# Performance work log

Hardware: AMD Instinct MI355X
Metric: run time of the kernel (lower is better)

## Reference

```python
import jax, jax.numpy as jnp
import numpy as np

EPS = 1e-5  # torch BatchNorm2d default


def _conv1x1(x, w):
    # x: [n, cin, h, w], w: [cout, cin] (1x1 conv == per-pixel matmul)
    return jnp.einsum('nchw,oc->nohw', x, w)


def _bn(x, gamma, beta, mean, var):
    # inference-mode BatchNorm2d over channel dim
    scale = gamma * jax.lax.rsqrt(var + EPS)
    shift = beta - mean * scale
    return x * scale[None, :, None, None] + shift[None, :, None, None]


def setup_inputs() -> dict:
    key = jax.random.key(0)
    ks = jax.random.split(key, 24)
    n, c, h, w = 16, 256, 64, 64
    width, planes = c // 2, c
    inp = {
        'x': jax.random.normal(ks[0], (n, c, h, w), jnp.float32),
        'w_theta': jax.random.normal(ks[1], (width, c), jnp.float32) * 0.05,
        'w_phi': jax.random.normal(ks[2], (width, c), jnp.float32) * 0.05,
        'w_g': jax.random.normal(ks[3], (width, c), jnp.float32) * 0.05,
        'w_zeta': jax.random.normal(ks[4], (planes, width), jnp.float32) * 0.05,
    }
    for i, (name, dim) in enumerate([('bn1', width), ('bn2', width), ('bn3', width), ('bn4', planes)]):
        k = 5 + 4 * i
        inp[f'{name}_gamma'] = jax.random.uniform(ks[k], (dim,), jnp.float32, 0.5, 1.5)
        inp[f'{name}_beta'] = jax.random.normal(ks[k + 1], (dim,), jnp.float32) * 0.1
        inp[f'{name}_mean'] = jax.random.normal(ks[k + 2], (dim,), jnp.float32) * 0.1
        inp[f'{name}_var'] = jax.random.uniform(ks[k + 3], (dim,), jnp.float32, 0.5, 1.5)
    return inp


def reference(x, w_theta, w_phi, w_g, w_zeta,
              bn1_gamma, bn1_beta, bn1_mean, bn1_var,
              bn2_gamma, bn2_beta, bn2_mean, bn2_var,
              bn3_gamma, bn3_beta, bn3_mean, bn3_var,
              bn4_gamma, bn4_beta, bn4_mean, bn4_var):
    n, c, h, w = x.shape
    theta = jax.nn.relu(_bn(_conv1x1(x, w_theta), bn1_gamma, bn1_beta, bn1_mean, bn1_var))
    phi = jax.nn.relu(_bn(_conv1x1(x, w_phi), bn2_gamma, bn2_beta, bn2_mean, bn2_var))
    g = jax.nn.relu(_bn(_conv1x1(x, w_g), bn3_gamma, bn3_beta, bn3_mean, bn3_var))

    width = theta.shape[1]
    hw = h * w
    theta = theta.reshape(n, width, hw)  # [n, C', S]
    phi = phi.reshape(n, width, hw)      # [n, C', S]
    g = g.reshape(n, width, hw)          # [n, C', S]

    # (theta^T @ phi) @ g^T == theta^T @ (phi @ g^T): no softmax, so associativity
    # lets us contract over pixels first -> O(S*C'^2) instead of O(S^2*C').
    kv = jnp.einsum('ncs,nds->ncd', phi, g)      # [n, C', C']
    out = jnp.einsum('ncs,ncd->nsd', theta, kv)  # [n, S, C']

    # faithful to torch: reshape (not transpose) [n, S, C'] -> [n, C', h, w]
    out = out.reshape(n, width, h, w)
    out = _bn(_conv1x1(out, w_zeta), bn4_gamma, bn4_beta, bn4_mean, bn4_var)
    return jax.nn.relu(out + x)
```

## Files before the change

### kernel.cpp

```cpp
#include <hip/hip_runtime.h>

#define BN_EPS 1e-5f

typedef unsigned short u16;
typedef __bf16 bf16x8 __attribute__((ext_vector_type(8)));
typedef float floatx4 __attribute__((ext_vector_type(4)));
typedef u16 u16x4 __attribute__((ext_vector_type(4)));
typedef u16 u16x8 __attribute__((ext_vector_type(8)));

__device__ __forceinline__ u16 f2bf(float f) {
    union { float f; unsigned int u; } v; v.f = f;
    unsigned int r = (v.u + 0x7fffu + ((v.u >> 16) & 1u)) >> 16;
    return (u16)r;
}

__device__ __forceinline__ void gld16(const void* gsrc, void* ldst) {
    __builtin_amdgcn_global_load_lds(
        (const __attribute__((address_space(1))) unsigned int*)gsrc,
        (__attribute__((address_space(3))) unsigned int*)ldst, 16, 0, 0);
}

__global__ __launch_bounds__(256) void prep_kernel(
    const float* __restrict__ wt, const float* __restrict__ wp,
    const float* __restrict__ wg, const float* __restrict__ wz,
    const float* __restrict__ g1, const float* __restrict__ b1,
    const float* __restrict__ m1, const float* __restrict__ v1,
    const float* __restrict__ g2, const float* __restrict__ b2,
    const float* __restrict__ m2, const float* __restrict__ v2,
    const float* __restrict__ g3, const float* __restrict__ b3,
    const float* __restrict__ m3, const float* __restrict__ v3,
    const float* __restrict__ g4, const float* __restrict__ b4,
    const float* __restrict__ m4, const float* __restrict__ v4,
    u16* __restrict__ W1bf, float* __restrict__ shift1,
    u16* __restrict__ Wzbf, float* __restrict__ shift4)
{
    int id = blockIdx.x * 256 + threadIdx.x;
    if (id < 384 * 256) {
        int r = id >> 8, c = id & 255;
        int grp = r >> 7, ch = r & 127;
        const float* wsrc = grp == 0 ? wt : (grp == 1 ? wp : wg);
        const float* gg = grp == 0 ? g1 : (grp == 1 ? g2 : g3);
        const float* bb = grp == 0 ? b1 : (grp == 1 ? b2 : b3);
        const float* mm = grp == 0 ? m1 : (grp == 1 ? m2 : m3);
        const float* vv = grp == 0 ? v1 : (grp == 1 ? v2 : v3);
        float scale = gg[ch] * rsqrtf(vv[ch] + BN_EPS);
        W1bf[id] = f2bf(wsrc[ch * 256 + c] * scale);
        if (c == 0) shift1[r] = bb[ch] - mm[ch] * scale;
    }
    if (id < 256 * 128) {
        int o = id >> 7;
        float scale = g4[o] * rsqrtf(v4[o] + BN_EPS);
        Wzbf[id] = f2bf(wz[id] * scale);
        if ((id & 127) == 0) shift4[o] = b4[o] - m4[o] * scale;
    }
}

__global__ __launch_bounds__(256) void xt_kernel(
    const float* __restrict__ x, u16* __restrict__ xt)
{
    const int stile = blockIdx.x, n = blockIdx.y;
    const int t = threadIdx.x;
    __shared__ __align__(16) u16 lds[64 * 256];

    const float* xb = x + (size_t)n * 1048576 + stile * 64;
    const int crow0 = t >> 4, sf4 = t & 15;
#pragma unroll
    for (int i = 0; i < 16; ++i) {
        int c = crow0 + 16 * i;
        float4 v = *((const float4*)(xb + (size_t)c * 4096) + sf4);
        int cseg = c >> 3, cin = c & 7;
#pragma unroll
        for (int j = 0; j < 4; ++j) {
            int s = sf4 * 4 + j;
            int csw = (cseg & ~7) | ((cseg ^ (s >> 2)) & 7);
            lds[s * 256 + csw * 8 + cin] = f2bf(((const float*)&v)[j]);
        }
    }
    __syncthreads();

    const int so = t >> 2, c4 = t & 3;
    u16* ob = xt + (size_t)n * 1048576 + (size_t)(stile * 64 + so) * 256;
#pragma unroll
    for (int i = 0; i < 8; ++i) {
        int cseg = c4 + 4 * i;
        int csw = (cseg & ~7) | ((cseg ^ (so >> 2)) & 7);
        *(u16x8*)(ob + cseg * 8) = *(const u16x8*)(lds + so * 256 + csw * 8);
    }
}

__global__ __launch_bounds__(256) void gemm1_kernel(
    const u16* __restrict__ xt, const u16* __restrict__ W1,
    const float* __restrict__ shift1,
    u16* __restrict__ theta_sm, u16* __restrict__ pg)
{
    const int st = blockIdx.x, mt = blockIdx.y, n = blockIdx.z;
    const int tid = threadIdx.x;
    const int w = tid >> 6, lane = tid & 63;
    const int quad = lane >> 4, l16 = lane & 15;

    __shared__ __align__(16) u16 ldsA[128 * 64];
    __shared__ __align__(16) u16 ldsB[128 * 64];

    floatx4 acc[2][8];
#pragma unroll
    for (int i = 0; i < 2; ++i)
#pragma unroll
        for (int j = 0; j < 8; ++j) acc[i][j] = floatx4{0.f, 0.f, 0.f, 0.f};

    const u16* xb = xt + (size_t)n * 1048576 + (size_t)st * 128 * 256;

    for (int kc = 0; kc < 4; ++kc) {
#pragma unroll
        for (int i = 0; i < 4; ++i) {
            int op = w * 4 + i;
            int r = op * 8 + (lane >> 3);
            int lseg = (lane & 7) ^ (r & 7);
            gld16(W1 + (size_t)(mt * 128 + r) * 256 + kc * 64 + lseg * 8,
                  ldsA + op * 512);
            gld16(xb + (size_t)r * 256 + kc * 64 + lseg * 8,
                  ldsB + op * 512);
        }
        __syncthreads();

#pragma unroll
        for (int kk = 0; kk < 2; ++kk) {
            bf16x8 a[2];
#pragma unroll
            for (int mi = 0; mi < 2; ++mi) {
                int r = w * 32 + mi * 16 + l16;
                int phys = (kk * 4 + quad) ^ (r & 7);
                a[mi] = *(const bf16x8*)(ldsA + r * 64 + phys * 8);
            }
#pragma unroll
            for (int ni = 0; ni < 8; ++ni) {
                int s = ni * 16 + l16;
                int phys = (kk * 4 + quad) ^ (s & 7);
                bf16x8 b = *(const bf16x8*)(ldsB + s * 64 + phys * 8);
#pragma unroll
                for (int mi = 0; mi < 2; ++mi)
                    acc[mi][ni] = __builtin_amdgcn_mfma_f32_16x16x32_bf16(
                        a[mi], b, acc[mi][ni], 0, 0, 0);
            }
        }
        __syncthreads();
    }

    if (mt == 0) {
#pragma unroll
        for (int mi = 0; mi < 2; ++mi) {
            int ocb = w * 32 + mi * 16 + quad * 4;
            float sh0 = shift1[ocb + 0], sh1 = shift1[ocb + 1];
            float sh2 = shift1[ocb + 2], sh3 = shift1[ocb + 3];
#pragma unroll
            for (int ni = 0; ni < 8; ++ni) {
                int s = st * 128 + ni * 16 + l16;
                float v0 = acc[mi][ni][0] + sh0, v1 = acc[mi][ni][1] + sh1;
                float v2 = acc[mi][ni][2] + sh2, v3 = acc[mi][ni][3] + sh3;
                u16x4 pk;
                pk[0] = f2bf(v0 > 0.f ? v0 : 0.f);
                pk[1] = f2bf(v1 > 0.f ? v1 : 0.f);
                pk[2] = f2bf(v2 > 0.f ? v2 : 0.f);
                pk[3] = f2bf(v3 > 0.f ? v3 : 0.f);
                *(u16x4*)(theta_sm + (size_t)n * 524288 + (size_t)s * 128 + ocb) = pk;
            }
        }
    } else {
#pragma unroll
        for (int mi = 0; mi < 2; ++mi)
#pragma unroll
            for (int r = 0; r < 4; ++r) {
                int oc = mt * 128 + w * 32 + mi * 16 + quad * 4 + r;
                int prow = (mt - 1) * 128 + w * 32 + mi * 16 + quad * 4 + r;
                float sh = shift1[oc];
#pragma unroll
                for (int ni = 0; ni < 8; ++ni) {
                    int s = st * 128 + ni * 16 + l16;
                    float val = acc[mi][ni][r] + sh;
                    val = val > 0.f ? val : 0.f;
                    pg[(size_t)n * 1048576 + (size_t)prow * 4096 + s] = f2bf(val);
                }
            }
    }
}

__global__ __launch_bounds__(256) void gemm2_kernel(
    const u16* __restrict__ pg, float* __restrict__ partials)
{
    const int kc = blockIdx.x, n = blockIdx.y;
    const int tid = threadIdx.x;
    const int w = tid >> 6, lane = tid & 63;
    const int quad = lane >> 4, l16 = lane & 15;

    __shared__ __align__(16) u16 ldsG[128 * 64];
    __shared__ __align__(16) u16 ldsP[128 * 64];

    floatx4 acc[2][8];
#pragma unroll
    for (int i = 0; i < 2; ++i)
#pragma unroll
        for (int j = 0; j < 8; ++j) acc[i][j] = floatx4{0.f, 0.f, 0.f, 0.f};

    const u16* base = pg + (size_t)n * 1048576;

    for (int ch = 0; ch < 2; ++ch) {
        int s0 = kc * 128 + ch * 64;
#pragma unroll
        for (int i = 0; i < 4; ++i) {
            int op = w * 4 + i;
            int r = op * 8 + (lane >> 3);
            int lseg = (lane & 7) ^ (r & 7);
            gld16(base + (size_t)(128 + r) * 4096 + s0 + lseg * 8, ldsG + op * 512);
            gld16(base + (size_t)r * 4096 + s0 + lseg * 8, ldsP + op * 512);
        }
        __syncthreads();

#pragma unroll
        for (int kk = 0; kk < 2; ++kk) {
            bf16x8 a[2];
#pragma unroll
            for (int mi = 0; mi < 2; ++mi) {
                int r = w * 32 + mi * 16 + l16;
                int phys = (kk * 4 + quad) ^ (r & 7);
                a[mi] = *(const bf16x8*)(ldsG + r * 64 + phys * 8);
            }
#pragma unroll
            for (int ci = 0; ci < 8; ++ci) {
                int r = ci * 16 + l16;
                int phys = (kk * 4 + quad) ^ (r & 7);
                bf16x8 b = *(const bf16x8*)(ldsP + r * 64 + phys * 8);
#pragma unroll
                for (int mi = 0; mi < 2; ++mi)
                    acc[mi][ci] = __builtin_amdgcn_mfma_f32_16x16x32_bf16(
                        a[mi], b, acc[mi][ci], 0, 0, 0);
            }
        }
        __syncthreads();
    }

    float* outp = partials + (size_t)(n * 32 + kc) * 16384;
#pragma unroll
    for (int mi = 0; mi < 2; ++mi)
#pragma unroll
        for (int r = 0; r < 4; ++r) {
            int d = w * 32 + mi * 16 + quad * 4 + r;
#pragma unroll
            for (int ci = 0; ci < 8; ++ci)
                outp[d * 128 + ci * 16 + l16] = acc[mi][ci][r];
        }
}

__global__ __launch_bounds__(256) void kv_reduce_kernel(
    const float* __restrict__ partials, u16* __restrict__ kvT)
{
    int n = blockIdx.y;
    int f4 = blockIdx.x * 256 + threadIdx.x;
    const float4* p4 = (const float4*)partials;
    float4 s = {0.f, 0.f, 0.f, 0.f};
#pragma unroll
    for (int kc = 0; kc < 32; ++kc) {
        float4 v = p4[(size_t)(n * 32 + kc) * 4096 + f4];
        s.x += v.x; s.y += v.y; s.z += v.z; s.w += v.w;
    }
    u16x4 o; o[0] = f2bf(s.x); o[1] = f2bf(s.y); o[2] = f2bf(s.z); o[3] = f2bf(s.w);
    *(u16x4*)(kvT + (size_t)n * 16384 + f4 * 4) = o;
}

__global__ __launch_bounds__(256) void gemm3_kernel(
    const u16* __restrict__ theta_sm, const u16* __restrict__ kvT,
    u16* __restrict__ out_sd)
{
    const int st = blockIdx.x, n = blockIdx.y;
    const int tid = threadIdx.x;
    const int w = tid >> 6, lane = tid & 63;
    const int quad = lane >> 4, l16 = lane & 15;

    __shared__ __align__(16) u16 ldsT[128 * 64];
    __shared__ __align__(16) u16 ldsK[128 * 64];

    floatx4 acc[2][8];
#pragma unroll
    for (int i = 0; i < 2; ++i)
#pragma unroll
        for (int j = 0; j < 8; ++j) acc[i][j] = floatx4{0.f, 0.f, 0.f, 0.f};

    const u16* tbase = theta_sm + (size_t)n * 524288 + (size_t)st * 128 * 128;
    const u16* kbase = kvT + (size_t)n * 16384;

    for (int ch = 0; ch < 2; ++ch) {
#pragma unroll
        for (int i = 0; i < 4; ++i) {
            int op = w * 4 + i;
            int r = op * 8 + (lane >> 3);
            int lseg = (lane & 7) ^ (r & 7);
            gld16(tbase + (size_t)r * 128 + ch * 64 + lseg * 8, ldsT + op * 512);
            gld16(kbase + (size_t)r * 128 + ch * 64 + lseg * 8, ldsK + op * 512);
        }
        __syncthreads();

#pragma unroll
        for (int kk = 0; kk < 2; ++kk) {
            bf16x8 a[2];
#pragma unroll
            for (int mi = 0; mi < 2; ++mi) {
                int r = w * 32 + mi * 16 + l16;
                int phys = (kk * 4 + quad) ^ (r & 7);
                a[mi] = *(const bf16x8*)(ldsT + r * 64 + phys * 8);
            }
#pragma unroll
            for (int di = 0; di < 8; ++di) {
                int r = di * 16 + l16;
                int phys = (kk * 4 + quad) ^ (r & 7);
                bf16x8 b = *(const bf16x8*)(ldsK + r * 64 + phys * 8);
#pragma unroll
                for (int mi = 0; mi < 2; ++mi)
                    acc[mi][di] = __builtin_amdgcn_mfma_f32_16x16x32_bf16(
                        a[mi], b, acc[mi][di], 0, 0, 0);
            }
        }
        __syncthreads();
    }

#pragma unroll
    for (int mi = 0; mi < 2; ++mi)
#pragma unroll
        for (int r = 0; r < 4; ++r) {
            int s = st * 128 + w * 32 + mi * 16 + quad * 4 + r;
#pragma unroll
            for (int di = 0; di < 8; ++di)
                out_sd[(size_t)n * 524288 + (size_t)s * 128 + di * 16 + l16] =
                    f2bf(acc[mi][di][r]);
        }
}

__device__ __forceinline__ int addsw(int seg, int s) {
    return (seg + (s & 7) + ((s >> 3) & 7)) & 7;
}

__global__ __launch_bounds__(256) void gemm4_kernel(
    const u16* __restrict__ out_sd, const u16* __restrict__ Wz,
    const float* __restrict__ shift4, const float* __restrict__ x,
    float* __restrict__ out)
{
    const int st = blockIdx.x, ot = blockIdx.y, n = blockIdx.z;
    const int tid = threadIdx.x;
    const int w = tid >> 6, lane = tid & 63;
    const int quad = lane >> 4, l16 = lane & 15;

    __shared__ __align__(16) u16 ldsY[128 * 64];
    __shared__ __align__(16) u16 ldsW[128 * 64];

    floatx4 acc[2][8];
#pragma unroll
    for (int i = 0; i < 2; ++i)
#pragma unroll
        for (int j = 0; j < 8; ++j) acc[i][j] = floatx4{0.f, 0.f, 0.f, 0.f};

    const int sl = tid & 15;
    const int cg = tid >> 4;
    const u16* ybase = out_sd + (size_t)n * 524288 + st * 128;
    unsigned int* ldsYdw = (unsigned int*)ldsY;

    u16x8 yv0[2], yv1[2];
#pragma unroll
    for (int p = 0; p < 2; ++p) {
        int c0 = 2 * cg + 32 * p;
        yv0[p] = *(const u16x8*)(ybase + (size_t)c0 * 4096 + 8 * sl);
        yv1[p] = *(const u16x8*)(ybase + (size_t)(c0 + 1) * 4096 + 8 * sl);
    }

    for (int kc = 0; kc < 2; ++kc) {
#pragma unroll
        for (int p = 0; p < 2; ++p) {
            int cp = cg + 16 * p, slog = cp >> 2, dwin = cp & 3;
#pragma unroll
            for (int j = 0; j < 8; ++j) {
                int s = 8 * sl + j;
                unsigned int pk = (unsigned int)yv0[p][j] | ((unsigned int)yv1[p][j] << 16);
                ldsYdw[s * 32 + addsw(slog, s) * 4 + dwin] = pk;
            }
        }
#pragma unroll
        for (int i = 0; i < 4; ++i) {
            int op = w * 4 + i;
            int r = op * 8 + (lane >> 3);
            int lseg = (lane & 7) ^ (r & 7);
            gld16(Wz + (size_t)(ot * 128 + r) * 128 + kc * 64 + lseg * 8, ldsW + op * 512);
        }
        if (kc < 1) {
#pragma unroll
            for (int p = 0; p < 2; ++p) {
                int c0 = 2 * cg + 32 * p;
                yv0[p] = *(const u16x8*)(ybase + (size_t)(64 + c0) * 4096 + 8 * sl);
                yv1[p] = *(const u16x8*)(ybase + (size_t)(64 + c0 + 1) * 4096 + 8 * sl);
            }
        }
        __syncthreads();

#pragma unroll
        for (int kk = 0; kk < 2; ++kk) {
            bf16x8 a[2];
#pragma unroll
            for (int mi = 0; mi < 2; ++mi) {
                int r = w * 32 + mi * 16 + l16;
                int phys = (kk * 4 + quad) ^ (r & 7);
                a[mi] = *(const bf16x8*)(ldsW + r * 64 + phys * 8);
            }
#pragma unroll
            for (int ni = 0; ni < 8; ++ni) {
                int s = ni * 16 + l16;
                int phys = addsw(kk * 4 + quad, s);
                bf16x8 b = *(const bf16x8*)(ldsY + s * 64 + phys * 8);
#pragma unroll
                for (int mi = 0; mi < 2; ++mi)
                    acc[mi][ni] = __builtin_amdgcn_mfma_f32_16x16x32_bf16(
                        a[mi], b, acc[mi][ni], 0, 0, 0);
            }
        }
        __syncthreads();
    }

#pragma unroll
    for (int mi = 0; mi < 2; ++mi)
#pragma unroll
        for (int r = 0; r < 4; ++r) {
            int o = ot * 128 + w * 32 + mi * 16 + quad * 4 + r;
            float sh = shift4[o];
#pragma unroll
            for (int ni = 0; ni < 8; ++ni) {
                int s2 = st * 128 + ni * 16 + l16;
                size_t idx = ((size_t)n * 256 + o) * 4096 + s2;
                float val = acc[mi][ni][r] + sh + x[idx];
                out[idx] = val > 0.f ? val : 0.f;
            }
        }
}

extern "C" void kernel_launch(void* const* d_in, const int* in_sizes, int n_in,
                              void* d_out, int out_size, void* d_ws, size_t ws_size,
                              hipStream_t stream)
{
    const float* x  = (const float*)d_in[0];
    const float* wt = (const float*)d_in[1];
    const float* wp = (const float*)d_in[2];
    const float* wg = (const float*)d_in[3];
    const float* wz = (const float*)d_in[4];
    const float* bn[16];
    for (int i = 0; i < 16; ++i) bn[i] = (const float*)d_in[5 + i];

    char* ws = (char*)d_ws;
    u16*   W1bf     = (u16*)  (ws + 0);
    float* shift1   = (float*)(ws + 196608);
    u16*   Wzbf     = (u16*)  (ws + 198144);
    float* shift4   = (float*)(ws + 263680);
    u16*   xt       = (u16*)  (ws + 264704);
    float* partials = (float*)(ws + 264704);
    u16*   theta_sm = (u16*)  (ws + 33819136);
    u16*   pg       = (u16*)  (ws + 50596352);
    u16*   out_sd   = (u16*)  (ws + 50596352);
    u16*   kvT      = (u16*)  (ws + 84150784 - 524288);
    float* out = (float*)d_out;

    prep_kernel<<<384, 256, 0, stream>>>(
        wt, wp, wg, wz,
        bn[0], bn[1], bn[2], bn[3],
        bn[4], bn[5], bn[6], bn[7],
        bn[8], bn[9], bn[10], bn[11],
        bn[12], bn[13], bn[14], bn[15],
        W1bf, shift1, Wzbf, shift4);

    xt_kernel<<<dim3(64, 16), 256, 0, stream>>>(x, xt);
    gemm1_kernel<<<dim3(32, 3, 16), 256, 0, stream>>>(xt, W1bf, shift1, theta_sm, pg);
    gemm2_kernel<<<dim3(32, 16), 256, 0, stream>>>(pg, partials);
    kv_reduce_kernel<<<dim3(16, 16), 256, 0, stream>>>(partials, kvT);
    gemm3_kernel<<<dim3(32, 16), 256, 0, stream>>>(theta_sm, kvT, out_sd);
    gemm4_kernel<<<dim3(32, 2, 16), 256, 0, stream>>>(out_sd, Wzbf, shift4, x, out);
}
```

Before: 234.1 us.

## Fuse gemm1 output tiles per block, shrink gemm2 split, single-stage gemm3

gemm1 now computes all three weight groups (theta, phi, g) in one block, so each x tile is loaded once rather than three times, at the cost of 96 accumulator vectors per thread, a larger LDS footprint and a 3x smaller grid. gemm2 covers 512 pixels per block instead of 128, so there are 8 partials per batch and less reduction traffic in kv_reduce. gemm3 loads the full K=128 tile in one pass with a 16-way swizzle, which drops one barrier round. The main risks are register pressure in gemm1 and lower parallelism (512 blocks for gemm1, 128 for gemm2).

```diff
diff --git a/kernel.cpp b/kernel.cpp
--- a/kernel.cpp
+++ b/kernel.cpp
@@ -88,83 +88,101 @@
     }
 }
 
-__global__ __launch_bounds__(256) void gemm1_kernel(
+__global__ __launch_bounds__(256, 2) void gemm1_kernel(
     const u16* __restrict__ xt, const u16* __restrict__ W1,
     const float* __restrict__ shift1,
     u16* __restrict__ theta_sm, u16* __restrict__ pg)
 {
-    const int st = blockIdx.x, mt = blockIdx.y, n = blockIdx.z;
+    const int st = blockIdx.x, n = blockIdx.y;
     const int tid = threadIdx.x;
     const int w = tid >> 6, lane = tid & 63;
     const int quad = lane >> 4, l16 = lane & 15;
 
-    __shared__ __align__(16) u16 ldsA[128 * 64];
+    __shared__ __align__(16) u16 ldsA[384 * 64];
     __shared__ __align__(16) u16 ldsB[128 * 64];
 
-    floatx4 acc[2][8];
-#pragma unroll
-    for (int i = 0; i < 2; ++i)
-#pragma unroll
-        for (int j = 0; j < 8; ++j) acc[i][j] = floatx4{0.f, 0.f, 0.f, 0.f};
+    floatx4 acc[3][2][8];
+#pragma unroll
+    for (int m = 0; m < 3; ++m)
+#pragma unroll
+        for (int i = 0; i < 2; ++i)
+#pragma unroll
+            for (int j = 0; j < 8; ++j) acc[m][i][j] = floatx4{0.f, 0.f, 0.f, 0.f};
 
     const u16* xb = xt + (size_t)n * 1048576 + (size_t)st * 128 * 256;
 
     for (int kc = 0; kc < 4; ++kc) {
+#pragma unroll
+        for (int i = 0; i < 12; ++i) {
+            int op = w * 12 + i;
+            int r = op * 8 + (lane >> 3);
+            int lseg = (lane & 7) ^ (r & 7);
+            gld16(W1 + (size_t)r * 256 + kc * 64 + lseg * 8, ldsA + op * 512);
+        }
 #pragma unroll
         for (int i = 0; i < 4; ++i) {
             int op = w * 4 + i;
             int r = op * 8 + (lane >> 3);
             int lseg = (lane & 7) ^ (r & 7);
-            gld16(W1 + (size_t)(mt * 128 + r) * 256 + kc * 64 + lseg * 8,
-                  ldsA + op * 512);
-            gld16(xb + (size_t)r * 256 + kc * 64 + lseg * 8,
-                  ldsB + op * 512);
+            gld16(xb + (size_t)r * 256 + kc * 64 + lseg * 8, ldsB + op * 512);
         }
         __syncthreads();
 
 #pragma unroll
         for (int kk = 0; kk < 2; ++kk) {
-            bf16x8 a[2];
-#pragma unroll
-            for (int mi = 0; mi < 2; ++mi) {
-                int r = w * 32 + mi * 16 + l16;
-                int phys = (kk * 4 + quad) ^ (r & 7);
-                a[mi] = *(const bf16x8*)(ldsA + r * 64 + phys * 8);
-            }
-#pragma unroll
-            for (int ni = 0; ni < 8; ++ni) {
-                int s = ni * 16 + l16;
-                int phys = (kk * 4 + quad) ^ (s & 7);
-                bf16x8 b = *(const bf16x8*)(ldsB + s * 64 + phys * 8);
-#pragma unroll
-                for (int mi = 0; mi < 2; ++mi)
-                    acc[mi][ni] = __builtin_amdgcn_mfma_f32_16x16x32_bf16(
-                        a[mi], b, acc[mi][ni], 0, 0, 0);
-            }
-        }
-        __syncthreads();
-    }
-
-    if (mt == 0) {
-#pragma unroll
-        for (int mi = 0; mi < 2; ++mi) {
-            int ocb = w * 32 + mi * 16 + quad * 4;
-            float sh0 = shift1[ocb + 0], sh1 = shift1[ocb + 1];
-            float sh2 = shift1[ocb + 2], sh3 = shift1[ocb + 3];
-#pragma unroll
-            for (int ni = 0; ni < 8; ++ni) {
-                int s = st * 128 + ni * 16 + l16;
-                float v0 = acc[mi][ni][0] + sh0, v1 = acc[mi][ni][1] + sh1;
-                float v2 = acc[mi][ni][2] + sh2, v3 = acc[mi][ni][3] + sh3;
-                u16x4 pk;
-                pk[0] = f2bf(v0 > 0.f ? v0 : 0.f);
-                pk[1] = f2bf(v1 > 0.f ? v1 : 0.f);
-                pk[2] = f2bf(v2 > 0.f ? v2 : 0.f);
-                pk[3] = f2bf(v3 > 0.f ? v3 : 0.f);
-                *(u16x4*)(theta_sm + (size_t)n * 524288 + (size_t)s * 128 + ocb) = pk;
-            }
-        }
-    } else {
+#pragma unroll
+            for (int g = 0; g < 2; ++g) {
+                bf16x8 b[4];
+#pragma unroll
+                for (int nj = 0; nj < 4; ++nj) {
+                    int s = (g * 4 + nj) * 16 + l16;
+                    int phys = (kk * 4 + quad) ^ (s & 7);
+                    b[nj] = *(const bf16x8*)(ldsB + s * 64 + phys * 8);
+                }
+#pragma unroll
+                for (int mt = 0; mt < 3; ++mt) {
+                    bf16x8 a0, a1;
+                    {
+                        int r = mt * 128 + w * 32 + l16;
+                        int phys = (kk * 4 + quad) ^ (r & 7);
+                        a0 = *(const bf16x8*)(ldsA + r * 64 + phys * 8);
+                        int r2 = r + 16;
+                        int phys2 = (kk * 4 + quad) ^ (r2 & 7);
+                        a1 = *(const bf16x8*)(ldsA + r2 * 64 + phys2 * 8);
+                    }
+#pragma unroll
+                    for (int nj = 0; nj < 4; ++nj) {
+                        acc[mt][0][g * 4 + nj] = __builtin_amdgcn_mfma_f32_16x16x32_bf16(
+                            a0, b[nj], acc[mt][0][g * 4 + nj], 0, 0, 0);
+                        acc[mt][1][g * 4 + nj] = __builtin_amdgcn_mfma_f32_16x16x32_bf16(
+                            a1, b[nj], acc[mt][1][g * 4 + nj], 0, 0, 0);
+                    }
+                }
+            }
+        }
+        __syncthreads();
+    }
+
+#pragma unroll
+    for (int mi = 0; mi < 2; ++mi) {
+        int ocb = w * 32 + mi * 16 + quad * 4;
+        float sh0 = shift1[ocb + 0], sh1 = shift1[ocb + 1];
+        float sh2 = shift1[ocb + 2], sh3 = shift1[ocb + 3];
+#pragma unroll
+        for (int ni = 0; ni < 8; ++ni) {
+            int s = st * 128 + ni * 16 + l16;
+            float v0 = acc[0][mi][ni][0] + sh0, v1 = acc[0][mi][ni][1] + sh1;
+            float v2 = acc[0][mi][ni][2] + sh2, v3 = acc[0][mi][ni][3] + sh3;
+            u16x4 pk;
+            pk[0] = f2bf(v0 > 0.f ? v0 : 0.f);
+            pk[1] = f2bf(v1 > 0.f ? v1 : 0.f);
+            pk[2] = f2bf(v2 > 0.f ? v2 : 0.f);
+            pk[3] = f2bf(v3 > 0.f ? v3 : 0.f);
+            *(u16x4*)(theta_sm + (size_t)n * 524288 + (size_t)s * 128 + ocb) = pk;
+        }
+    }
+#pragma unroll
+    for (int mt = 1; mt < 3; ++mt)
 #pragma unroll
         for (int mi = 0; mi < 2; ++mi)
 #pragma unroll
@@ -175,12 +193,11 @@
 #pragma unroll
                 for (int ni = 0; ni < 8; ++ni) {
                     int s = st * 128 + ni * 16 + l16;
-                    float val = acc[mi][ni][r] + sh;
+                    float val = acc[mt][mi][ni][r] + sh;
                     val = val > 0.f ? val : 0.f;
                     pg[(size_t)n * 1048576 + (size_t)prow * 4096 + s] = f2bf(val);
                 }
             }
-    }
 }
 
 __global__ __launch_bounds__(256) void gemm2_kernel(
@@ -202,8 +219,8 @@
 
     const u16* base = pg + (size_t)n * 1048576;
 
-    for (int ch = 0; ch < 2; ++ch) {
-        int s0 = kc * 128 + ch * 64;
+    for (int ch = 0; ch < 8; ++ch) {
+        int s0 = kc * 512 + ch * 64;
 #pragma unroll
         for (int i = 0; i < 4; ++i) {
             int op = w * 4 + i;
@@ -237,7 +254,7 @@
         __syncthreads();
     }
 
-    float* outp = partials + (size_t)(n * 32 + kc) * 16384;
+    float* outp = partials + (size_t)(n * 8 + kc) * 16384;
 #pragma unroll
     for (int mi = 0; mi < 2; ++mi)
 #pragma unroll
@@ -257,8 +274,8 @@
     const float4* p4 = (const float4*)partials;
     float4 s = {0.f, 0.f, 0.f, 0.f};
 #pragma unroll
-    for (int kc = 0; kc < 32; ++kc) {
-        float4 v = p4[(size_t)(n * 32 + kc) * 4096 + f4];
+    for (int kc = 0; kc < 8; ++kc) {
+        float4 v = p4[(size_t)(n * 8 + kc) * 4096 + f4];
         s.x += v.x; s.y += v.y; s.z += v.z; s.w += v.w;
     }
     u16x4 o; o[0] = f2bf(s.x); o[1] = f2bf(s.y); o[2] = f2bf(s.z); o[3] = f2bf(s.w);
@@ -274,8 +291,8 @@
     const int w = tid >> 6, lane = tid & 63;
     const int quad = lane >> 4, l16 = lane & 15;
 
-    __shared__ __align__(16) u16 ldsT[128 * 64];
-    __shared__ __align__(16) u16 ldsK[128 * 64];
+    __shared__ __align__(16) u16 ldsT[128 * 128];
+    __shared__ __align__(16) u16 ldsK[128 * 128];
 
     floatx4 acc[2][8];
 #pragma unroll
@@ -286,38 +303,35 @@
     const u16* tbase = theta_sm + (size_t)n * 524288 + (size_t)st * 128 * 128;
     const u16* kbase = kvT + (size_t)n * 16384;
 
-    for (int ch = 0; ch < 2; ++ch) {
-#pragma unroll
-        for (int i = 0; i < 4; ++i) {
-            int op = w * 4 + i;
-            int r = op * 8 + (lane >> 3);
-            int lseg = (lane & 7) ^ (r & 7);
-            gld16(tbase + (size_t)r * 128 + ch * 64 + lseg * 8, ldsT + op * 512);
-            gld16(kbase + (size_t)r * 128 + ch * 64 + lseg * 8, ldsK + op * 512);
-        }
-        __syncthreads();
-
-#pragma unroll
-        for (int kk = 0; kk < 2; ++kk) {
-            bf16x8 a[2];
-#pragma unroll
-            for (int mi = 0; mi < 2; ++mi) {
-                int r = w * 32 + mi * 16 + l16;
-                int phys = (kk * 4 + quad) ^ (r & 7);
-                a[mi] = *(const bf16x8*)(ldsT + r * 64 + phys * 8);
-            }
-#pragma unroll
-            for (int di = 0; di < 8; ++di) {
-                int r = di * 16 + l16;
-                int phys = (kk * 4 + quad) ^ (r & 7);
-                bf16x8 b = *(const bf16x8*)(ldsK + r * 64 + phys * 8);
-#pragma unroll
-                for (int mi = 0; mi < 2; ++mi)
-                    acc[mi][di] = __builtin_amdgcn_mfma_f32_16x16x32_bf16(
-                        a[mi], b, acc[mi][di], 0, 0, 0);
-            }
-        }
-        __syncthreads();
+#pragma unroll
+    for (int i = 0; i < 8; ++i) {
+        int op = w * 8 + i;
+        int r = op * 4 + (lane >> 4);
+        int g = (lane & 15) ^ (r & 15);
+        gld16(tbase + (size_t)r * 128 + g * 8, ldsT + op * 512);
+        gld16(kbase + (size_t)r * 128 + g * 8, ldsK + op * 512);
+    }
+    __syncthreads();
+
+#pragma unroll
+    for (int kk = 0; kk < 4; ++kk) {
+        bf16x8 a[2];
+#pragma unroll
+        for (int mi = 0; mi < 2; ++mi) {
+            int r = w * 32 + mi * 16 + l16;
+            int phys = (kk * 4 + quad) ^ (r & 15);
+            a[mi] = *(const bf16x8*)(ldsT + r * 128 + phys * 8);
+        }
+#pragma unroll
+        for (int di = 0; di < 8; ++di) {
+            int r = di * 16 + l16;
+            int phys = (kk * 4 + quad) ^ (r & 15);
+            bf16x8 b = *(const bf16x8*)(ldsK + r * 128 + phys * 8);
+#pragma unroll
+            for (int mi = 0; mi < 2; ++mi)
+                acc[mi][di] = __builtin_amdgcn_mfma_f32_16x16x32_bf16(
+                    a[mi], b, acc[mi][di], 0, 0, 0);
+        }
     }
 
 #pragma unroll
@@ -469,8 +483,8 @@
         W1bf, shift1, Wzbf, shift4);
 
     xt_kernel<<<dim3(64, 16), 256, 0, stream>>>(x, xt);
-    gemm1_kernel<<<dim3(32, 3, 16), 256, 0, stream>>>(xt, W1bf, shift1, theta_sm, pg);
-    gemm2_kernel<<<dim3(32, 16), 256, 0, stream>>>(pg, partials);
+    gemm1_kernel<<<dim3(32, 16), 256, 0, stream>>>(xt, W1bf, shift1, theta_sm, pg);
+    gemm2_kernel<<<dim3(8, 16), 256, 0, stream>>>(pg, partials);
     kv_reduce_kernel<<<dim3(16, 16), 256, 0, stream>>>(partials, kvT);
     gemm3_kernel<<<dim3(32, 16), 256, 0, stream>>>(theta_sm, kvT, out_sd);
     gemm4_kernel<<<dim3(32, 2, 16), 256, 0, stream>>>(out_sd, Wzbf, shift4, x, out);
```

Measured after the change: 254.9 us. +8.9%, slower.
